# Kernel tuning notes

Measured on AMD Instinct MI355X. Metric: run time of the kernel, lower is better.

The kernel has to match this reference:

```python
import jax, jax.numpy as jnp
import numpy as np
from jax import lax

B, C_IN, C_OUT, H, W = 32, 64, 128, 112, 112
EPS = 1e-5
DW_THRESH = 4.0
PW_THRESH = 0.001


def setup_inputs() -> dict:
    key = jax.random.key(0)
    ks = jax.random.split(key, 13)
    inp = {
        "x": jax.random.normal(ks[0], (B, C_IN, H, W), jnp.float32) * 2.0,
        "dw_w": jax.random.normal(ks[1], (C_IN, 1, 3, 3), jnp.float32) * 0.3,
        "dw_b": jax.random.normal(ks[2], (C_IN,), jnp.float32) * 0.1,
        "bn1_g": jax.random.uniform(ks[3], (C_IN,), jnp.float32, 0.5, 3.5),
        "bn1_b": jax.random.normal(ks[4], (C_IN,), jnp.float32) * 0.1,
        "bn1_m": jax.random.normal(ks[5], (C_IN,), jnp.float32) * 0.1,
        "bn1_v": jax.random.uniform(ks[6], (C_IN,), jnp.float32, 0.5, 1.5),
        "pw_w": jax.random.normal(ks[7], (C_OUT, C_IN), jnp.float32) * 0.1,
        "pw_b": jax.random.normal(ks[8], (C_OUT,), jnp.float32) * 0.1,
        "bn2_g": jax.random.uniform(ks[9], (C_OUT,), jnp.float32, 0.5, 1.5),
        "bn2_b": jax.random.normal(ks[10], (C_OUT,), jnp.float32) * 0.1,
        "bn2_m": jax.random.normal(ks[11], (C_OUT,), jnp.float32) * 0.1,
        "bn2_v": jax.random.uniform(ks[12], (C_OUT,), jnp.float32, 0.5, 1.5),
    }
    return inp


def _bn(x, g, b, m, v):
    # inference-mode BatchNorm2d over channel axis 1
    inv = g * lax.rsqrt(v + EPS)
    return x * inv[None, :, None, None] + (b - m * inv)[None, :, None, None]


def _channel_cut(x, thresh):
    # zero each (batch, channel) plane whose max |value| over HxW is < thresh
    max_abs = jnp.max(jnp.abs(x), axis=(2, 3), keepdims=True)  # [B, C, 1, 1]
    return jnp.where(max_abs < thresh, 0.0, x)


def reference(x, dw_w, dw_b, bn1_g, bn1_b, bn1_m, bn1_v,
              pw_w, pw_b, bn2_g, bn2_b, bn2_m, bn2_v):
    # depthwise 3x3 conv, padding=1, groups=C_IN
    y = lax.conv_general_dilated(
        x, dw_w, window_strides=(1, 1), padding=[(1, 1), (1, 1)],
        dimension_numbers=("NCHW", "OIHW", "NCHW"),
        feature_group_count=C_IN)
    y = y + dw_b[None, :, None, None]
    y = jax.nn.relu(_bn(y, bn1_g, bn1_b, bn1_m, bn1_v))
    y = _channel_cut(y, DW_THRESH)
    # pointwise 1x1 conv == channel contraction
    z = jnp.einsum("bchw,oc->bohw", y, pw_w) + pw_b[None, :, None, None]
    z = jax.nn.relu(_bn(z, bn2_g, bn2_b, bn2_m, bn2_v))
    z = _channel_cut(z, PW_THRESH)
    return z
```

## Files before the change

### kernel.cpp

```cpp
#include <hip/hip_runtime.h>
#include <hip/hip_bf16.h>

#define EPS 1e-5f
#define DW_THRESH 4.0f
#define PW_THRESH 0.001f

typedef __bf16 bf16x4 __attribute__((ext_vector_type(4)));
typedef __bf16 bf16x8 __attribute__((ext_vector_type(8)));
typedef float f32x4 __attribute__((ext_vector_type(4)));

__global__ __launch_bounds__(256, 4) void k_dw(
    const float* __restrict__ x, const float* __restrict__ dww, const float* __restrict__ dwb,
    const float* __restrict__ g1, const float* __restrict__ b1,
    const float* __restrict__ m1, const float* __restrict__ v1,
    const float* __restrict__ zp,
    __bf16* __restrict__ ybuf, unsigned* __restrict__ flags_y)
{
    __shared__ float xs[4][19][128];
    __shared__ float wsc[4][9];
    __shared__ float bi1s[4];

    const int s   = blockIdx.x;
    const int cg  = blockIdx.y;
    const int b   = blockIdx.z;
    const int tid = threadIdx.x;
    const int h0  = s * 16;

    if (tid < 36) {
        int c = tid / 9, k = tid % 9;
        int ch = cg * 4 + c;
        float inv = g1[ch] * rsqrtf(v1[ch] + EPS);
        wsc[c][k] = dww[ch * 9 + k] * inv;
        if (k == 0) bi1s[c] = dwb[ch] * inv + b1[ch] - m1[ch] * inv;
    }
    if (tid < 16) xs[tid >> 2][0][124 + (tid & 3)] = 0.f;

    const int lane  = tid & 63;
    const int wid   = tid >> 6;
    const int lane5 = lane & 31;
    const int half  = lane >> 5;
    const float* xc_base = x + ((long)(b * 64 + cg * 4) * 12544);
#pragma unroll
    for (int issue = 0; issue < 9; ++issue) {
        int rowIdx0 = issue * 8 + wid * 2;
        int c0 = rowIdx0 / 18;
        int j0 = rowIdx0 - c0 * 18;
        int h  = h0 - 1 + j0 + half;
        const float* src = ((unsigned)h < 112u && lane5 < 28)
            ? (xc_base + c0 * 12544 + h * 112 + lane5 * 4)
            : (zp + lane5 * 4);
        __builtin_amdgcn_global_load_lds(
            (const __attribute__((address_space(1))) void*)src,
            (__attribute__((address_space(3))) void*)(&xs[c0][1 + j0][0]),
            16, 0, 0);
    }
    __syncthreads();

    float cmax[4] = {0.f, 0.f, 0.f, 0.f};
    const int hwbase = h0 * 112;

#pragma unroll
    for (int it = 0; it < 2; ++it) {
        int qid = it * 256 + tid;
        if (qid >= 448) break;
        int r  = qid / 28;
        int w0 = (qid - r * 28) * 4;

        float yv[4][4];
#pragma unroll
        for (int c = 0; c < 4; ++c) {
            float a0 = 0.f, a1 = 0.f, a2 = 0.f, a3 = 0.f;
#pragma unroll
            for (int dh = 0; dh < 3; ++dh) {
                const float* row = &xs[c][1 + r + dh][0];
                f32x4 A = *reinterpret_cast<const f32x4*>(row + w0 - 4);
                f32x4 B = *reinterpret_cast<const f32x4*>(row + w0);
                f32x4 C = *reinterpret_cast<const f32x4*>(row + w0 + 4);
                float k0 = wsc[c][dh * 3 + 0];
                float k1 = wsc[c][dh * 3 + 1];
                float k2 = wsc[c][dh * 3 + 2];
                a0 = fmaf(k0, A[3], fmaf(k1, B[0], fmaf(k2, B[1], a0)));
                a1 = fmaf(k0, B[0], fmaf(k1, B[1], fmaf(k2, B[2], a1)));
                a2 = fmaf(k0, B[1], fmaf(k1, B[2], fmaf(k2, B[3], a2)));
                a3 = fmaf(k0, B[2], fmaf(k1, B[3], fmaf(k2, C[0], a3)));
            }
            float bi = bi1s[c];
            yv[c][0] = fmaxf(a0 + bi, 0.f);
            yv[c][1] = fmaxf(a1 + bi, 0.f);
            yv[c][2] = fmaxf(a2 + bi, 0.f);
            yv[c][3] = fmaxf(a3 + bi, 0.f);
            cmax[c] = fmaxf(cmax[c],
                      fmaxf(fmaxf(yv[c][0], yv[c][1]), fmaxf(yv[c][2], yv[c][3])));
        }

        int hw    = hwbase + r * 112 + w0;
        int hwblk = hw >> 4;
        int l16   = hw & 15;
        long base = (((long)(b * 784 + hwblk) * 16 + cg) * 16 + l16) * 4;
        bf16x8 pk0 = { (__bf16)yv[0][0], (__bf16)yv[1][0], (__bf16)yv[2][0], (__bf16)yv[3][0],
                       (__bf16)yv[0][1], (__bf16)yv[1][1], (__bf16)yv[2][1], (__bf16)yv[3][1] };
        bf16x8 pk1 = { (__bf16)yv[0][2], (__bf16)yv[1][2], (__bf16)yv[2][2], (__bf16)yv[3][2],
                       (__bf16)yv[0][3], (__bf16)yv[1][3], (__bf16)yv[2][3], (__bf16)yv[3][3] };
        *reinterpret_cast<bf16x8*>(ybuf + base)     = pk0;
        *reinterpret_cast<bf16x8*>(ybuf + base + 8) = pk1;
    }

#pragma unroll
    for (int c = 0; c < 4; ++c) {
        float m = cmax[c];
#pragma unroll
        for (int d = 1; d < 64; d <<= 1)
            m = fmaxf(m, __shfl_xor(m, d, 64));
        if (lane == 0)
            atomicMax(&flags_y[b * 64 + cg * 4 + c], __float_as_uint(m));
    }
}

__global__ __launch_bounds__(256) void k_pw(
    const float* __restrict__ pww, const float* __restrict__ pwb,
    const float* __restrict__ g2, const float* __restrict__ b2,
    const float* __restrict__ m2, const float* __restrict__ v2,
    const __bf16* __restrict__ ybuf, const unsigned* __restrict__ flags_y,
    float* __restrict__ out, unsigned* __restrict__ flags_z)
{
    __shared__ __bf16 wl[128][72];
    __shared__ float s2[128], bb2[128];
    __shared__ float keepf[64];
    __shared__ unsigned pmz[128];

    const int t   = blockIdx.x;
    const int b   = blockIdx.y;
    const int tid = threadIdx.x;
    const int hw0 = t * 128;

    if (tid < 64)
        keepf[tid] = (__uint_as_float(flags_y[b * 64 + tid]) < DW_THRESH) ? 0.f : 1.f;
    if (tid < 128) {
        float inv = g2[tid] * rsqrtf(v2[tid] + EPS);
        s2[tid]  = inv;
        bb2[tid] = pwb[tid] * inv + b2[tid] - m2[tid] * inv;
        pmz[tid] = 0u;
    }
    __syncthreads();
    for (int i = tid; i < 8192; i += 256) {
        int o = i >> 6, c = i & 63;
        wl[o][c] = (__bf16)(pww[i] * keepf[c]);
    }
    __syncthreads();

    const int wid = tid >> 6, lane = tid & 63;
    const int wm = wid >> 1, wn = wid & 1;
    const int g = lane >> 4, l16 = lane & 15;

    bf16x8 af[4][2];
#pragma unroll
    for (int m = 0; m < 4; ++m)
#pragma unroll
        for (int kb = 0; kb < 2; ++kb)
            af[m][kb] = *reinterpret_cast<const bf16x8*>(&wl[64 * wm + 16 * m + l16][32 * kb + 8 * g]);

    bf16x8 bfr[4][2];
    const int hwblk0 = (hw0 >> 4) + 4 * wn;
#pragma unroll
    for (int q = 0; q < 4; ++q)
#pragma unroll
        for (int kb = 0; kb < 2; ++kb) {
            long rb = ((long)(b * 784 + hwblk0 + q)) * 16;
            int grp = kb * 8 + 2 * g;
            bf16x4 lo = *reinterpret_cast<const bf16x4*>(ybuf + (rb + grp)     * 64 + l16 * 4);
            bf16x4 hi = *reinterpret_cast<const bf16x4*>(ybuf + (rb + grp + 1) * 64 + l16 * 4);
            bfr[q][kb] = (bf16x8){ lo[0], lo[1], lo[2], lo[3],
                                   hi[0], hi[1], hi[2], hi[3] };
        }

    f32x4 acc[4][4];
#pragma unroll
    for (int m = 0; m < 4; ++m)
#pragma unroll
        for (int q = 0; q < 4; ++q)
            acc[m][q] = (f32x4){0.f, 0.f, 0.f, 0.f};

#pragma unroll
    for (int kb = 0; kb < 2; ++kb)
#pragma unroll
        for (int m = 0; m < 4; ++m)
#pragma unroll
            for (int q = 0; q < 4; ++q)
                acc[m][q] = __builtin_amdgcn_mfma_f32_16x16x32_bf16(
                    af[m][kb], bfr[q][kb], acc[m][q], 0, 0, 0);

#pragma unroll
    for (int m = 0; m < 4; ++m) {
#pragma unroll
        for (int r = 0; r < 4; ++r) {
            int o = 64 * wm + 16 * m + 4 * g + r;
            float sc = s2[o], bi = bb2[o];
            float mx = 0.f;
#pragma unroll
            for (int q = 0; q < 4; ++q) {
                float val = fmaxf(fmaf(acc[m][q][r], sc, bi), 0.f);
                mx = fmaxf(mx, val);
                out[(b * 128 + o) * 12544 + hw0 + 64 * wn + 16 * q + l16] = val;
            }
#pragma unroll
            for (int d = 1; d < 16; d <<= 1)
                mx = fmaxf(mx, __shfl_xor(mx, d, 64));
            if (l16 == 0)
                atomicMax(&pmz[o], __float_as_uint(mx));
        }
    }
    __syncthreads();
    if (tid < 128)
        atomicMax(&flags_z[b * 128 + tid], pmz[tid]);
}

__global__ __launch_bounds__(256) void k_cut(
    const unsigned* __restrict__ flags_z, float* __restrict__ out)
{
    int p = blockIdx.x;
    if (__uint_as_float(flags_z[p]) >= PW_THRESH) return;
    int base = p * 12544;
    for (int i = threadIdx.x; i < 12544; i += 256)
        out[base + i] = 0.f;
}

extern "C" void kernel_launch(void* const* d_in, const int* in_sizes, int n_in,
                              void* d_out, int out_size, void* d_ws, size_t ws_size,
                              hipStream_t stream)
{
    const float* x   = (const float*)d_in[0];
    const float* dww = (const float*)d_in[1];
    const float* dwb = (const float*)d_in[2];
    const float* g1  = (const float*)d_in[3];
    const float* b1  = (const float*)d_in[4];
    const float* m1  = (const float*)d_in[5];
    const float* v1  = (const float*)d_in[6];
    const float* pww = (const float*)d_in[7];
    const float* pwb = (const float*)d_in[8];
    const float* g2  = (const float*)d_in[9];
    const float* b2  = (const float*)d_in[10];
    const float* m2  = (const float*)d_in[11];
    const float* v2  = (const float*)d_in[12];
    float* out = (float*)d_out;

    unsigned char* ws = (unsigned char*)d_ws;
    unsigned* flags_y = (unsigned*)ws;
    unsigned* flags_z = (unsigned*)(ws + 8192);
    const float* zp   = (const float*)(ws + 24576);
    __bf16* ybuf      = (__bf16*)(ws + 65536);

    hipMemsetAsync(ws, 0, 25600, stream);

    dim3 gdw(7, 16, 32);
    k_dw<<<gdw, 256, 0, stream>>>(x, dww, dwb, g1, b1, m1, v1, zp, ybuf, flags_y);

    dim3 gpw(98, 32);
    k_pw<<<gpw, 256, 0, stream>>>(pww, pwb, g2, b2, m2, v2, ybuf, flags_y, out, flags_z);

    k_cut<<<4096, 256, 0, stream>>>(flags_z, out);
}
```

Before: 117.1 us.

## Halve depthwise row tile, vectorize weight staging, and transpose MFMA output for float4 stores

The depthwise kernel now handles 8 rows per block instead of 16. That doubles the grid and shrinks shared memory, so more blocks fit per CU (launch bounds raised to 7), at the cost of more halo reloads. In the pointwise kernel the MFMA operands are swapped so each lane holds 4 consecutive spatial outputs for one channel. This allows 128-bit float4 stores to the output and a shorter max-reduction shuffle. The pointwise weight staging is also vectorized into float4 loads and bf16x4 shared stores.

Measured after the change: 134.8 us. 15.1% more time.

```diff
diff --git a/kernel.cpp b/kernel.cpp
--- a/kernel.cpp
+++ b/kernel.cpp
@@ -9,14 +9,14 @@
 typedef __bf16 bf16x8 __attribute__((ext_vector_type(8)));
 typedef float f32x4 __attribute__((ext_vector_type(4)));
 
-__global__ __launch_bounds__(256, 4) void k_dw(
+__global__ __launch_bounds__(256, 7) void k_dw(
     const float* __restrict__ x, const float* __restrict__ dww, const float* __restrict__ dwb,
     const float* __restrict__ g1, const float* __restrict__ b1,
     const float* __restrict__ m1, const float* __restrict__ v1,
     const float* __restrict__ zp,
     __bf16* __restrict__ ybuf, unsigned* __restrict__ flags_y)
 {
-    __shared__ float xs[4][19][128];
+    __shared__ float xs[4][11][128];
     __shared__ float wsc[4][9];
     __shared__ float bi1s[4];
 
@@ -24,7 +24,7 @@
     const int cg  = blockIdx.y;
     const int b   = blockIdx.z;
     const int tid = threadIdx.x;
-    const int h0  = s * 16;
+    const int h0  = s * 8;
 
     if (tid < 36) {
         int c = tid / 9, k = tid % 9;
@@ -41,10 +41,10 @@
     const int half  = lane >> 5;
     const float* xc_base = x + ((long)(b * 64 + cg * 4) * 12544);
 #pragma unroll
-    for (int issue = 0; issue < 9; ++issue) {
+    for (int issue = 0; issue < 5; ++issue) {
         int rowIdx0 = issue * 8 + wid * 2;
-        int c0 = rowIdx0 / 18;
-        int j0 = rowIdx0 - c0 * 18;
+        int c0 = rowIdx0 / 10;
+        int j0 = rowIdx0 - c0 * 10;
         int h  = h0 - 1 + j0 + half;
         const float* src = ((unsigned)h < 112u && lane5 < 28)
             ? (xc_base + c0 * 12544 + h * 112 + lane5 * 4)
@@ -59,12 +59,9 @@
     float cmax[4] = {0.f, 0.f, 0.f, 0.f};
     const int hwbase = h0 * 112;
 
-#pragma unroll
-    for (int it = 0; it < 2; ++it) {
-        int qid = it * 256 + tid;
-        if (qid >= 448) break;
-        int r  = qid / 28;
-        int w0 = (qid - r * 28) * 4;
+    if (tid < 224) {
+        const int r  = tid / 28;
+        const int w0 = (tid - r * 28) * 4;
 
         float yv[4][4];
 #pragma unroll
@@ -73,16 +70,16 @@
 #pragma unroll
             for (int dh = 0; dh < 3; ++dh) {
                 const float* row = &xs[c][1 + r + dh][0];
-                f32x4 A = *reinterpret_cast<const f32x4*>(row + w0 - 4);
-                f32x4 B = *reinterpret_cast<const f32x4*>(row + w0);
-                f32x4 C = *reinterpret_cast<const f32x4*>(row + w0 + 4);
+                f32x4 A  = *reinterpret_cast<const f32x4*>(row + w0 - 4);
+                f32x4 Bv = *reinterpret_cast<const f32x4*>(row + w0);
+                f32x4 Cv = *reinterpret_cast<const f32x4*>(row + w0 + 4);
                 float k0 = wsc[c][dh * 3 + 0];
                 float k1 = wsc[c][dh * 3 + 1];
                 float k2 = wsc[c][dh * 3 + 2];
-                a0 = fmaf(k0, A[3], fmaf(k1, B[0], fmaf(k2, B[1], a0)));
-                a1 = fmaf(k0, B[0], fmaf(k1, B[1], fmaf(k2, B[2], a1)));
-                a2 = fmaf(k0, B[1], fmaf(k1, B[2], fmaf(k2, B[3], a2)));
-                a3 = fmaf(k0, B[2], fmaf(k1, B[3], fmaf(k2, C[0], a3)));
+                a0 = fmaf(k0, A[3],  fmaf(k1, Bv[0], fmaf(k2, Bv[1], a0)));
+                a1 = fmaf(k0, Bv[0], fmaf(k1, Bv[1], fmaf(k2, Bv[2], a1)));
+                a2 = fmaf(k0, Bv[1], fmaf(k1, Bv[2], fmaf(k2, Bv[3], a2)));
+                a3 = fmaf(k0, Bv[2], fmaf(k1, Bv[3], fmaf(k2, Cv[0], a3)));
             }
             float bi = bi1s[c];
             yv[c][0] = fmaxf(a0 + bi, 0.f);
@@ -97,12 +94,12 @@
         int hwblk = hw >> 4;
         int l16   = hw & 15;
         long base = (((long)(b * 784 + hwblk) * 16 + cg) * 16 + l16) * 4;
-        bf16x8 pk0 = { (__bf16)yv[0][0], (__bf16)yv[1][0], (__bf16)yv[2][0], (__bf16)yv[3][0],
-                       (__bf16)yv[0][1], (__bf16)yv[1][1], (__bf16)yv[2][1], (__bf16)yv[3][1] };
-        bf16x8 pk1 = { (__bf16)yv[0][2], (__bf16)yv[1][2], (__bf16)yv[2][2], (__bf16)yv[3][2],
-                       (__bf16)yv[0][3], (__bf16)yv[1][3], (__bf16)yv[2][3], (__bf16)yv[3][3] };
-        *reinterpret_cast<bf16x8*>(ybuf + base)     = pk0;
-        *reinterpret_cast<bf16x8*>(ybuf + base + 8) = pk1;
+        bf16x8 p0 = { (__bf16)yv[0][0], (__bf16)yv[1][0], (__bf16)yv[2][0], (__bf16)yv[3][0],
+                      (__bf16)yv[0][1], (__bf16)yv[1][1], (__bf16)yv[2][1], (__bf16)yv[3][1] };
+        bf16x8 p1 = { (__bf16)yv[0][2], (__bf16)yv[1][2], (__bf16)yv[2][2], (__bf16)yv[3][2],
+                      (__bf16)yv[0][3], (__bf16)yv[1][3], (__bf16)yv[2][3], (__bf16)yv[3][3] };
+        *reinterpret_cast<bf16x8*>(ybuf + base)     = p0;
+        *reinterpret_cast<bf16x8*>(ybuf + base + 8) = p1;
     }
 
 #pragma unroll
@@ -142,9 +139,20 @@
         pmz[tid] = 0u;
     }
     __syncthreads();
-    for (int i = tid; i < 8192; i += 256) {
-        int o = i >> 6, c = i & 63;
-        wl[o][c] = (__bf16)(pww[i] * keepf[c]);
+    {
+        const f32x4* pw4 = reinterpret_cast<const f32x4*>(pww);
+#pragma unroll
+        for (int k = 0; k < 8; ++k) {
+            int i = k * 256 + tid;
+            f32x4 wv = pw4[i];
+            int o  = i >> 4;
+            int c4 = (i & 15) << 2;
+            bf16x4 bv = { (__bf16)(wv[0] * keepf[c4 + 0]),
+                          (__bf16)(wv[1] * keepf[c4 + 1]),
+                          (__bf16)(wv[2] * keepf[c4 + 2]),
+                          (__bf16)(wv[3] * keepf[c4 + 3]) };
+            *reinterpret_cast<bf16x4*>(&wl[o][c4]) = bv;
+        }
     }
     __syncthreads();
 
@@ -187,27 +195,28 @@
 #pragma unroll
             for (int q = 0; q < 4; ++q)
                 acc[m][q] = __builtin_amdgcn_mfma_f32_16x16x32_bf16(
-                    af[m][kb], bfr[q][kb], acc[m][q], 0, 0, 0);
+                    bfr[q][kb], af[m][kb], acc[m][q], 0, 0, 0);
 
 #pragma unroll
     for (int m = 0; m < 4; ++m) {
-#pragma unroll
-        for (int r = 0; r < 4; ++r) {
-            int o = 64 * wm + 16 * m + 4 * g + r;
-            float sc = s2[o], bi = bb2[o];
-            float mx = 0.f;
-#pragma unroll
-            for (int q = 0; q < 4; ++q) {
-                float val = fmaxf(fmaf(acc[m][q][r], sc, bi), 0.f);
-                mx = fmaxf(mx, val);
-                out[(b * 128 + o) * 12544 + hw0 + 64 * wn + 16 * q + l16] = val;
+        int o = 64 * wm + 16 * m + l16;
+        float sc = s2[o], bi = bb2[o];
+        float mx = 0.f;
+        long pbase = (long)(b * 128 + o) * 12544 + hw0 + 64 * wn + 4 * g;
+#pragma unroll
+        for (int q = 0; q < 4; ++q) {
+            f32x4 v;
+#pragma unroll
+            for (int r = 0; r < 4; ++r) {
+                v[r] = fmaxf(fmaf(acc[m][q][r], sc, bi), 0.f);
+                mx = fmaxf(mx, v[r]);
             }
-#pragma unroll
-            for (int d = 1; d < 16; d <<= 1)
-                mx = fmaxf(mx, __shfl_xor(mx, d, 64));
-            if (l16 == 0)
-                atomicMax(&pmz[o], __float_as_uint(mx));
-        }
+            *reinterpret_cast<f32x4*>(out + pbase + 16 * q) = v;
+        }
+        mx = fmaxf(mx, __shfl_xor(mx, 16, 64));
+        mx = fmaxf(mx, __shfl_xor(mx, 32, 64));
+        if (lane < 16)
+            atomicMax(&pmz[o], __float_as_uint(mx));
     }
     __syncthreads();
     if (tid < 128)
@@ -251,7 +260,7 @@
 
     hipMemsetAsync(ws, 0, 25600, stream);
 
-    dim3 gdw(7, 16, 32);
+    dim3 gdw(14, 16, 32);
     k_dw<<<gdw, 256, 0, stream>>>(x, dww, dwb, g1, b1, m1, v1, zp, ybuf, flags_y);
 
     dim3 gpw(98, 32);
```
